# Kernel optimization log

Hardware: AMD Instinct MI355X
Metric: run time of the kernel (lower is better)

The kernel has to match this reference:

```python
import jax, jax.numpy as jnp
import numpy as np

E = 256   # embed_size
H = 256   # hidden_size
C = 3     # channels
V = 257   # pixel vocab (0..255 + boundary token 256)
B, R, CO = 128, 32, 32


def setup_inputs() -> dict:
    key = jax.random.key(0)
    ks = jax.random.split(key, 16)
    s = 0.05
    return {
        "x": jax.random.randint(ks[0], (B, C, R, CO), 0, V),
        "emb": jax.random.normal(ks[1], (C, V, E), dtype=jnp.float32) * s,
        "xcomb_W": jax.random.normal(ks[2], (C, E, 2 * E), dtype=jnp.float32) * s,
        "xcomb_b": jax.random.normal(ks[3], (C, E), dtype=jnp.float32) * s,
        "hcomb_W": jax.random.normal(ks[4], (C, H, 2 * H), dtype=jnp.float32) * s,
        "hcomb_b": jax.random.normal(ks[5], (C, H), dtype=jnp.float32) * s,
        "W_ih": jax.random.normal(ks[6], (C, 3 * H, E + 2), dtype=jnp.float32) * s,
        "W_hh": jax.random.normal(ks[7], (C, 3 * H, H), dtype=jnp.float32) * s,
        "b_ih": jax.random.normal(ks[8], (C, 3 * H), dtype=jnp.float32) * s,
        "b_hh": jax.random.normal(ks[9], (C, 3 * H), dtype=jnp.float32) * s,
        "red_W": jax.random.normal(ks[10], (V, H), dtype=jnp.float32) * s,
        "red_b": jax.random.normal(ks[11], (V,), dtype=jnp.float32) * s,
        "green_W": jax.random.normal(ks[12], (V, H + E), dtype=jnp.float32) * s,
        "green_b": jax.random.normal(ks[13], (V,), dtype=jnp.float32) * s,
        "blue_W": jax.random.normal(ks[14], (V, H + 2 * E), dtype=jnp.float32) * s,
        "blue_b": jax.random.normal(ks[15], (V,), dtype=jnp.float32) * s,
    }


def _forward(x, emb, xcomb_W, xcomb_b, hcomb_W, hcomb_b, W_ih, W_hh, b_ih, b_hh,
             red_W, red_b, green_W, green_b, blue_W, blue_b):
    Bb, Cc, Rr, Co = x.shape
    Nr, Nc = Rr - 1, Co - 1
    Hd = W_hh.shape[-1]
    dt = emb.dtype

    # context pixel indices for each output position (row+1,col+1)
    left = x[:, :, 1:, :-1]    # x[:,c,row+1,col]
    above = x[:, :, :-1, 1:]   # x[:,c,row,col+1]
    target = x[:, :, 1:, 1:]   # x[:,c,row+1,col+1] (conditioning embeds for green/blue)

    # per-channel embedding gather, vectorized over all positions
    gather = jax.vmap(lambda t, idx: t[idx], in_axes=(0, 1), out_axes=1)
    left_e = gather(emb, left)      # [B,C,Nr,Nc,E]
    above_e = gather(emb, above)
    target_e = gather(emb, target)

    # x_comb linear on cat(left,above); hidden-independent -> precompute
    xi = jnp.concatenate([left_e, above_e], axis=-1)                     # [B,C,Nr,Nc,2E]
    xi = jnp.einsum('bcrke,cfe->bcrkf', xi, xcomb_W) + xcomb_b[None, :, None, None, :]

    # positional (row,col) features appended as floats (torch.cat promotion)
    pos_r = jnp.broadcast_to(jnp.arange(Nr, dtype=dt)[:, None], (Nr, Nc))
    pos_c = jnp.broadcast_to(jnp.arange(Nc, dtype=dt)[None, :], (Nr, Nc))
    pos = jnp.broadcast_to(jnp.stack([pos_r, pos_c], -1)[None, None], (Bb, Cc, Nr, Nc, 2))
    xfull = jnp.concatenate([xi, pos], axis=-1)                          # [B,C,Nr,Nc,E+2]

    # GRU input projection is hidden-independent -> precompute gates_x
    gx = jnp.einsum('bcrkf,cgf->bcrkg', xfull, W_ih) + b_ih[None, :, None, None, :]
    gx = jnp.transpose(gx, (2, 3, 1, 0, 4))                              # [Nr,Nc,C,B,3H]

    def col_step(prev_left, xs):
        gx_col, prev_row_col = xs   # [C,B,3H], [C,B,H]
        pl = prev_left              # [B,H], shared across channels and cols
        hs = []
        for c in range(Cc):         # fixed small channel loop (sequential dependence)
            hcat = jnp.concatenate([pl, prev_row_col[c]], axis=-1)       # [B,2H]
            h = hcat @ hcomb_W[c].T + hcomb_b[c]                          # [B,H]
            gh = h @ W_hh[c].T + b_hh[c]                                  # [B,3H]
            gxr, gxz, gxn = jnp.split(gx_col[c], 3, axis=-1)
            ghr, ghz, ghn = jnp.split(gh, 3, axis=-1)
            r = jax.nn.sigmoid(gxr + ghr)
            z = jax.nn.sigmoid(gxz + ghz)
            n = jnp.tanh(gxn + r * ghn)
            hnew = (1.0 - z) * n + z * h
            pl = hnew
            hs.append(hnew)
        return pl, jnp.stack(hs, 0)  # carry, [C,B,H]

    def row_step(prev_row, gx_row):
        # prev_row: hiddens from previous row [Nc,C,B,H]
        init_left = jnp.zeros((Bb, Hd), dtype=dt)
        _, hs_row = jax.lax.scan(col_step, init_left, (gx_row, prev_row))
        return hs_row, hs_row

    init_row = jnp.zeros((Nc, Cc, Bb, Hd), dtype=dt)
    _, h_all = jax.lax.scan(row_step, init_row, gx)   # [Nr,Nc,C,B,H]

    te = jnp.transpose(target_e, (2, 3, 1, 0, 4))     # [Nr,Nc,C,B,E]
    h0, h1, h2 = h_all[:, :, 0], h_all[:, :, 1], h_all[:, :, 2]  # [Nr,Nc,B,H]
    lr = h0 @ red_W.T + red_b
    lg = jnp.concatenate([h1, te[:, :, 0]], -1) @ green_W.T + green_b
    lb = jnp.concatenate([h2, te[:, :, 0], te[:, :, 1]], -1) @ blue_W.T + blue_b
    logits = jnp.stack([lr, lg, lb], 0)               # [C,Nr,Nc,B,V]
    return jnp.transpose(logits, (3, 0, 1, 2, 4))     # [B,C,Nr,Nc,V]


def reference(x, emb, xcomb_W, xcomb_b, hcomb_W, hcomb_b, W_ih, W_hh, b_ih, b_hh,
              red_W, red_b, green_W, green_b, blue_W, blue_b):
    return _forward(x, emb, xcomb_W, xcomb_b, hcomb_W, hcomb_b, W_ih, W_hh,
                    b_ih, b_hh, red_W, red_b, green_W, green_b, blue_W, blue_b)
```

## Files before the change

kernel.cpp:

```cpp
#include <hip/hip_runtime.h>

typedef __attribute__((ext_vector_type(4))) float f32x4;
typedef __attribute__((ext_vector_type(8))) short s16x8;
typedef unsigned long long u64;

__device__ __forceinline__ unsigned short f2bf(float f) {
  union { float f; unsigned u; } v; v.f = f;
  unsigned r = v.u + 0x7fffu + ((v.u >> 16) & 1u);
  return (unsigned short)(r >> 16);
}


__global__ void prep_wbig(const float* __restrict__ hcomb_W, const float* __restrict__ hcomb_b,
                          const float* __restrict__ W_hh, const float* __restrict__ b_hh,
                          unsigned short* __restrict__ Wbig, float* __restrict__ bbig) {
  __shared__ float red[256];
  const int c = blockIdx.x, g = blockIdx.y, t = threadIdx.x;
  const float* hW = hcomb_W + (size_t)c * 256 * 512;
  unsigned short* orow = Wbig + ((size_t)c * 1024 + g) * 512;
  if (g < 256) {
    orow[t]       = f2bf(hW[(size_t)g * 512 + t]);
    orow[t + 256] = f2bf(hW[(size_t)g * 512 + t + 256]);
    if (t == 0) bbig[c * 1024 + g] = hcomb_b[c * 256 + g];
    return;
  }
  const int gp = g - 256;
  const float* wrow = W_hh + ((size_t)c * 768 + gp) * 256;
  float a0 = 0.f, a1 = 0.f;
  for (int h = 0; h < 256; h++) {
    float w = wrow[h];
    a0 += w * hW[(size_t)h * 512 + t];
    a1 += w * hW[(size_t)h * 512 + t + 256];
  }
  orow[t] = f2bf(a0); orow[t + 256] = f2bf(a1);
  red[t] = wrow[t] * hcomb_b[c * 256 + t];
  __syncthreads();
  for (int s = 128; s > 0; s >>= 1) { if (t < s) red[t] += red[t + s]; __syncthreads(); }
  if (t == 0) bbig[c * 1024 + g] = red[0] + b_hh[c * 768 + gp];
}

__global__ void prep_u(const float* __restrict__ emb, const float* __restrict__ xcomb_W,
                       float* __restrict__ Ul, float* __restrict__ Ua) {
  __shared__ float er[256];
  const int c = blockIdx.x, v = blockIdx.y, side = blockIdx.z, f = threadIdx.x;
  er[f] = emb[((size_t)c * 257 + v) * 256 + f];
  __syncthreads();
  const float* wrow = xcomb_W + ((size_t)c * 256 + f) * 512 + side * 256;
  float a = 0.f;
  for (int e = 0; e < 256; e++) a += er[e] * wrow[e];
  (side ? Ua : Ul)[((size_t)c * 257 + v) * 256 + f] = a;
}

__global__ void prep_t(const float* __restrict__ W_ih, const float* __restrict__ Ul,
                       const float* __restrict__ Ua, float* __restrict__ Tl, float* __restrict__ Ta) {
  __shared__ float ur[256];
  const int c = blockIdx.x, v = blockIdx.y, side = blockIdx.z, g = threadIdx.x;
  if (g < 256) ur[g] = (side ? Ua : Ul)[((size_t)c * 257 + v) * 256 + g];
  __syncthreads();
  const float* wrow = W_ih + ((size_t)c * 768 + g) * 258;
  float a = 0.f;
  for (int f = 0; f < 256; f++) a += ur[f] * wrow[f];
  (side ? Ta : Tl)[((size_t)c * 257 + v) * 768 + g] = a;
}

__global__ void prep_bgx(const float* __restrict__ W_ih, const float* __restrict__ xcomb_b,
                         const float* __restrict__ b_ih, float* __restrict__ bgx) {
  __shared__ float xb[256];
  const int c = blockIdx.x, g = threadIdx.x;
  if (g < 256) xb[g] = xcomb_b[c * 256 + g];
  __syncthreads();
  const float* wrow = W_ih + ((size_t)c * 768 + g) * 258;
  float a = b_ih[c * 768 + g];
  for (int f = 0; f < 256; f++) a += xb[f] * wrow[f];
  bgx[c * 768 + g] = a;
}

__global__ void prep_tgb(const float* __restrict__ emb, const float* __restrict__ green_W,
                         const float* __restrict__ blue_W,
                         float* __restrict__ TG, float* __restrict__ TB0, float* __restrict__ TB1) {
  __shared__ float er[256];
  const int v = blockIdx.x, which = blockIdx.y, u = threadIdx.x;
  const int ch = (which == 2) ? 1 : 0;
  if (u < 256) er[u] = emb[((size_t)ch * 257 + v) * 256 + u];
  __syncthreads();
  if (u >= 257) return;
  const float* W; int pitch, off; float* T;
  if (which == 0)      { W = green_W; pitch = 512; off = 256; T = TG;  }
  else if (which == 1) { W = blue_W;  pitch = 768; off = 256; T = TB0; }
  else                 { W = blue_W;  pitch = 768; off = 512; T = TB1; }
  const float* wrow = W + (size_t)u * pitch + off;
  float a = 0.f;
  for (int e = 0; e < 256; e++) a += er[e] * wrow[e];
  T[(size_t)v * 257 + u] = a;
}

__global__ void prep_w3(const float* __restrict__ red_W, const float* __restrict__ green_W,
                        const float* __restrict__ blue_W, unsigned short* __restrict__ W3) {
  const int c = blockIdx.x, v = blockIdx.y, t = threadIdx.x;
  float val = 0.f;
  if (v < 257) {
    if (c == 0)      val = red_W[(size_t)v * 256 + t];
    else if (c == 1) val = green_W[(size_t)v * 512 + t];
    else             val = blue_W[(size_t)v * 768 + t];
  }
  W3[((size_t)c * 272 + v) * 256 + t] = f2bf(val);
}

__global__ void prep_gx(const int* __restrict__ x,
                        const float* __restrict__ Tl, const float* __restrict__ Ta,
                        const float* __restrict__ bgx, const float* __restrict__ bbig,
                        const float* __restrict__ W_ih, float* __restrict__ pregx) {
  __shared__ float base[768];
  __shared__ int ix0[128], ix1[128];
  const int r = blockIdx.x, k = blockIdx.y, c = blockIdx.z, tid = threadIdx.x;
  for (int g = tid; g < 768; g += 256) {
    float v = bgx[c * 768 + g]
            + (float)r * W_ih[((size_t)c * 768 + g) * 258 + 256]
            + (float)k * W_ih[((size_t)c * 768 + g) * 258 + 257];
    if (g < 512) v += bbig[c * 1024 + 256 + g];
    base[g] = v;
  }
  if (tid < 128) {
    ix0[tid] = x[((tid * 3 + c) * 32 + (r + 1)) * 32 + k];
    ix1[tid] = x[((tid * 3 + c) * 32 + r) * 32 + (k + 1)];
  }
  __syncthreads();
  const size_t cell = ((size_t)(r * 31 + k)) * 3 + c;
  float* outp = pregx + cell * 3 * 128 * 256;
  const float* Tlc = Tl + (size_t)c * 257 * 768;
  const float* Tac = Ta + (size_t)c * 257 * 768;
  #pragma unroll 2
  for (int b = 0; b < 128; ++b) {
    const float* tl = Tlc + (size_t)ix0[b] * 768;
    const float* ta = Tac + (size_t)ix1[b] * 768;
    #pragma unroll
    for (int q = 0; q < 3; ++q) {
      const int g = q * 256 + tid;
      outp[((size_t)q * 128 + b) * 256 + tid] = tl[g] + ta[g] + base[g];
    }
  }
}

__global__ void zero_flags(int* __restrict__ f, int n) {
  int i = blockIdx.x * 256 + threadIdx.x;
  if (i < n) f[i] = 0;
}


__device__ __forceinline__ void spinwait(int* f, int target) {
  while (__hip_atomic_load(f, __ATOMIC_RELAXED, __HIP_MEMORY_SCOPE_AGENT) < target)
    __builtin_amdgcn_s_sleep(2);
}

__global__ __launch_bounds__(256, 2)
void persist_kernel(const int* __restrict__ x, float* __restrict__ hbuf,
                    const unsigned short* __restrict__ Wbig, const float* __restrict__ bbig,
                    const float* __restrict__ pregx,
                    const unsigned short* __restrict__ W3,
                    const float* __restrict__ TG, const float* __restrict__ TB0,
                    const float* __restrict__ TB1,
                    const float* __restrict__ red_b, const float* __restrict__ green_b,
                    const float* __restrict__ blue_b,
                    float* __restrict__ out, int* __restrict__ flags)
{
  __shared__ unsigned short Abuf[128 * 136];
  __shared__ int idx0[128], idx1[128];

  const int id = blockIdx.x;
  const int rlo = id & 7, slot = id >> 3;
  const int rhi = slot / 5, role = slot - 5 * rhi;
  const int r = rlo + 8 * rhi;
  if (r > 30) return;

  int* sflag = flags;
  int* eflag = flags + 124 * 31;

  const int tid = threadIdx.x;
  const int lane = tid & 63, wv = tid >> 6;
  const int quad = lane >> 4, l16 = lane & 15;

  if (role < 4) {
    const int jcol = role * 64 + wv * 16;
    const int j = jcol + l16;

    for (int L = r; L <= r + 92; ++L) {
      const int t = L - r;
      const int k = t / 3, c = t - 3 * k;
      const size_t cell = ((size_t)(r * 31 + k)) * 3 + c;
      const float* pg = pregx + cell * 3 * 128 * 256;

      f32x4 acc[8][4];
      const float bh  = bbig[c * 1024 + j];
      const float bn3 = bbig[c * 1024 + 768 + j];
      #pragma unroll
      for (int mt = 0; mt < 8; ++mt)
        #pragma unroll
        for (int i = 0; i < 4; ++i) {
          const int b = mt * 16 + quad * 4 + i;
          acc[mt][0][i] = bh;
          acc[mt][1][i] = pg[(size_t)b * 256 + j];
          acc[mt][2][i] = pg[(size_t)(128 + b) * 256 + j];
          acc[mt][3][i] = bn3;
        }

      if (tid == 0) {
        if (t >= 1) spinwait(&sflag[(L - 1) * 31 + r], 4);
        if (r >= 1) spinwait(&sflag[(L - 1) * 31 + (r - 1)], 4);
        if (t >= 3) {
          if (r < 30) spinwait(&sflag[(L - 2) * 31 + (r + 1)], 4);
          spinwait(&eflag[(L - 2) * 31 + r], 1);
        }
      }
      __syncthreads();
      __builtin_amdgcn_fence(__ATOMIC_ACQUIRE, "agent");

      const bool pl_zero = (t == 0);
      const bool a_zero  = (r == 0);
      const float* plp = hbuf + ((size_t)(r * 3 + (c == 0 ? 2 : c - 1)) * 128) * 256;
      const float* ap  = (r > 0) ? hbuf + ((size_t)((r - 1) * 3 + c) * 128) * 256 : hbuf;
      const unsigned short* Wb = Wbig + (size_t)c * 1024 * 512;

      for (int kc = 0; kc < 4; ++kc) {
        const bool from_pl = (kc < 2);
        const float* src = from_pl ? plp : ap;
        const bool zero = from_pl ? pl_zero : a_zero;
        const int colbase = from_pl ? kc * 128 : (kc - 2) * 128;
        __syncthreads();
        #pragma unroll 8
        for (int it = 0; it < 16; ++it) {
          const int li = it * 256 + tid;
          const int row = li >> 5;
          const int col = (li & 31) * 4;
          unsigned short o0 = 0, o1 = 0, o2 = 0, o3 = 0;
          if (!zero) {
            const float4 v = *(const float4*)(src + (size_t)row * 256 + colbase + col);
            o0 = f2bf(v.x); o1 = f2bf(v.y); o2 = f2bf(v.z); o3 = f2bf(v.w);
          }
          unsigned short* d = &Abuf[row * 136 + col];
          d[0] = o0; d[1] = o1; d[2] = o2; d[3] = o3;
        }
        __syncthreads();
        #pragma unroll
        for (int ks = 0; ks < 4; ++ks) {
          const int kofs = ks * 32 + quad * 8;
          s16x8 bf[4];
          #pragma unroll
          for (int g = 0; g < 4; ++g)
            bf[g] = *(const s16x8*)(Wb + (size_t)(g * 256 + jcol + l16) * 512 + kc * 128 + kofs);
          #pragma unroll
          for (int mt = 0; mt < 8; ++mt) {
            const s16x8 af = *(const s16x8*)&Abuf[(mt * 16 + l16) * 136 + kofs];
            #pragma unroll
            for (int g = 0; g < 4; ++g)
              acc[mt][g] = __builtin_amdgcn_mfma_f32_16x16x32_bf16(af, bf[g], acc[mt][g], 0, 0, 0);
          }
        }
      }

      const float* pgn = pg + (size_t)2 * 128 * 256;
      float* hout = hbuf + ((size_t)(r * 3 + c) * 128) * 256;
      #pragma unroll
      for (int mt = 0; mt < 8; ++mt)
        #pragma unroll
        for (int i = 0; i < 4; ++i) {
          const int b = mt * 16 + quad * 4 + i;
          const float gxn = pgn[(size_t)b * 256 + j];
          const float h  = acc[mt][0][i];
          const float rg = __fdividef(1.f, 1.f + __expf(-acc[mt][1][i]));
          const float zg = __fdividef(1.f, 1.f + __expf(-acc[mt][2][i]));
          const float ng = 1.f - __fdividef(2.f, __expf(2.f * (gxn + rg * acc[mt][3][i])) + 1.f);
          hout[(size_t)b * 256 + j] = (1.f - zg) * ng + zg * h;
        }

      __syncthreads();
      if (tid == 0)
        __hip_atomic_fetch_add(&sflag[L * 31 + r], 1, __ATOMIC_RELEASE, __HIP_MEMORY_SCOPE_AGENT);
    }
  } else {
    for (int Le = r + 1; Le <= r + 93; ++Le) {
      const int t = Le - 1 - r;
      const int k = t / 3, c = t - 3 * k;

      if (tid == 0) spinwait(&sflag[(Le - 1) * 31 + r], 4);
      __syncthreads();
      __builtin_amdgcn_fence(__ATOMIC_ACQUIRE, "agent");

      if (tid < 128) {
        idx0[tid] = x[((tid * 3 + 0) * 32 + (r + 1)) * 32 + (k + 1)];
        idx1[tid] = x[((tid * 3 + 1) * 32 + (r + 1)) * 32 + (k + 1)];
      }

      const float* hsrc = hbuf + ((size_t)(r * 3 + c) * 128) * 256;
      const unsigned short* W3c = W3 + (size_t)c * 272 * 256;

      f32x4 acc[2][17];
      #pragma unroll
      for (int m2 = 0; m2 < 2; ++m2)
        #pragma unroll
        for (int nt = 0; nt < 17; ++nt)
          #pragma unroll
          for (int e = 0; e < 4; ++e) acc[m2][nt][e] = 0.f;

      for (int kc = 0; kc < 2; ++kc) {
        __syncthreads();
        #pragma unroll 8
        for (int it = 0; it < 16; ++it) {
          const int li = it * 256 + tid;
          const int row = li >> 5;
          const int col = (li & 31) * 4;
          const float4 v = *(const float4*)(hsrc + (size_t)row * 256 + kc * 128 + col);
          unsigned short* d = &Abuf[row * 136 + col];
          d[0] = f2bf(v.x); d[1] = f2bf(v.y); d[2] = f2bf(v.z); d[3] = f2bf(v.w);
        }
        __syncthreads();
        if (kc == 1 && tid == 0)
          __hip_atomic_fetch_add(&eflag[Le * 31 + r], 1, __ATOMIC_RELEASE, __HIP_MEMORY_SCOPE_AGENT);
        #pragma unroll
        for (int ks = 0; ks < 4; ++ks) {
          const int kofs = ks * 32 + quad * 8;
          s16x8 af[2];
          #pragma unroll
          for (int m2 = 0; m2 < 2; ++m2)
            af[m2] = *(const s16x8*)&Abuf[((wv * 2 + m2) * 16 + l16) * 136 + kofs];
          #pragma unroll
          for (int nt = 0; nt < 17; ++nt) {
            const s16x8 bf = *(const s16x8*)(W3c + (size_t)(nt * 16 + l16) * 256 + kc * 128 + kofs);
            #pragma unroll
            for (int m2 = 0; m2 < 2; ++m2)
              acc[m2][nt] = __builtin_amdgcn_mfma_f32_16x16x32_bf16(af[m2], bf, acc[m2][nt], 0, 0, 0);
          }
        }
      }

      const float* bias = (c == 0) ? red_b : (c == 1) ? green_b : blue_b;
      #pragma unroll
      for (int m2 = 0; m2 < 2; ++m2)
        #pragma unroll
        for (int i = 0; i < 4; ++i) {
          const int b = (m2 + wv * 2) * 16 + quad * 4 + i;
          const int t0 = idx0[b], t1 = idx1[b];
          float* orow = out + ((size_t)((b * 3 + c) * 31 + r) * 31 + k) * 257;
          #pragma unroll
          for (int nt = 0; nt < 17; ++nt) {
            const int v = nt * 16 + l16;
            if (v < 257) {
              float val = acc[m2][nt][i] + bias[v];
              if (c == 1)      val += TG[(size_t)t0 * 257 + v];
              else if (c == 2) val += TB0[(size_t)t0 * 257 + v] + TB1[(size_t)t1 * 257 + v];
              orow[v] = val;
            }
          }
        }
    }
  }
}


extern "C" void kernel_launch(void* const* d_in, const int* in_sizes, int n_in,
                              void* d_out, int out_size, void* d_ws, size_t ws_size,
                              hipStream_t stream) {
  const int*   x       = (const int*)  d_in[0];
  const float* emb     = (const float*)d_in[1];
  const float* xcomb_W = (const float*)d_in[2];
  const float* xcomb_b = (const float*)d_in[3];
  const float* hcomb_W = (const float*)d_in[4];
  const float* hcomb_b = (const float*)d_in[5];
  const float* W_ih    = (const float*)d_in[6];
  const float* W_hh    = (const float*)d_in[7];
  const float* b_ih    = (const float*)d_in[8];
  const float* b_hh    = (const float*)d_in[9];
  const float* red_W   = (const float*)d_in[10];
  const float* red_b   = (const float*)d_in[11];
  const float* green_W = (const float*)d_in[12];
  const float* green_b = (const float*)d_in[13];
  const float* blue_W  = (const float*)d_in[14];
  const float* blue_b  = (const float*)d_in[15];
  float* out = (float*)d_out;

  char* p = (char*)d_ws;
  auto alloc = [&](size_t bytes) -> char* {
    char* r = p; p += (bytes + 255) & ~(size_t)255; return r;
  };
  float* hbuf          = (float*)alloc((size_t)31 * 3 * 128 * 256 * 4);
  unsigned short* Wbig = (unsigned short*)alloc((size_t)3 * 1024 * 512 * 2);
  float* bbig          = (float*)alloc((size_t)3 * 1024 * 4);
  float* Tl            = (float*)alloc((size_t)3 * 257 * 768 * 4);
  float* Ta            = (float*)alloc((size_t)3 * 257 * 768 * 4);
  float* Ul            = (float*)alloc((size_t)3 * 257 * 256 * 4);
  float* Ua            = (float*)alloc((size_t)3 * 257 * 256 * 4);
  float* bgx           = (float*)alloc((size_t)3 * 768 * 4);
  unsigned short* W3   = (unsigned short*)alloc((size_t)3 * 272 * 256 * 2);
  float* TG            = (float*)alloc((size_t)257 * 257 * 4);
  float* TB0           = (float*)alloc((size_t)257 * 257 * 4);
  float* TB1           = (float*)alloc((size_t)257 * 257 * 4);
  int*   flags         = (int*)  alloc((size_t)2 * 124 * 31 * 4);
  float* pregx         = (float*)alloc((size_t)2883 * 3 * 128 * 256 * 4);

  prep_wbig<<<dim3(3, 1024), dim3(256), 0, stream>>>(hcomb_W, hcomb_b, W_hh, b_hh, Wbig, bbig);
  prep_u<<<dim3(3, 257, 2), dim3(256), 0, stream>>>(emb, xcomb_W, Ul, Ua);
  prep_t<<<dim3(3, 257, 2), dim3(768), 0, stream>>>(W_ih, Ul, Ua, Tl, Ta);
  prep_bgx<<<dim3(3), dim3(768), 0, stream>>>(W_ih, xcomb_b, b_ih, bgx);
  prep_tgb<<<dim3(257, 3), dim3(320), 0, stream>>>(emb, green_W, blue_W, TG, TB0, TB1);
  prep_w3<<<dim3(3, 272), dim3(256), 0, stream>>>(red_W, green_W, blue_W, W3);
  prep_gx<<<dim3(31, 31, 3), dim3(256), 0, stream>>>(x, Tl, Ta, bgx, bbig, W_ih, pregx);
  zero_flags<<<dim3(31), dim3(256), 0, stream>>>(flags, 2 * 124 * 31);

  persist_kernel<<<dim3(160), dim3(256), 0, stream>>>(
      x, hbuf, Wbig, bbig, pregx, W3, TG, TB0, TB1, red_b, green_b, blue_b, out, flags);
}
```

Baseline: 10.39 ms.

## Replace agent-scope acquire fences with coherent atomic loads of hidden states

New measurement: 9.559 ms. -8.0%, faster.

```diff
diff --git a/kernel.cpp b/kernel.cpp
--- a/kernel.cpp
+++ b/kernel.cpp
@@ -152,6 +152,10 @@
     __builtin_amdgcn_s_sleep(2);
 }
 
+__device__ __forceinline__ u64 load_coh(const float* p) {
+  return __hip_atomic_load((const u64*)p, __ATOMIC_RELAXED, __HIP_MEMORY_SCOPE_SYSTEM);
+}
+
 __global__ __launch_bounds__(256, 2)
 void persist_kernel(const int* __restrict__ x, float* __restrict__ hbuf,
                     const unsigned short* __restrict__ Wbig, const float* __restrict__ bbig,
@@ -212,7 +216,7 @@
         }
       }
       __syncthreads();
-      __builtin_amdgcn_fence(__ATOMIC_ACQUIRE, "agent");
+      __builtin_amdgcn_fence(__ATOMIC_ACQUIRE, "workgroup");
 
       const bool pl_zero = (t == 0);
       const bool a_zero  = (r == 0);
@@ -231,13 +235,17 @@
           const int li = it * 256 + tid;
           const int row = li >> 5;
           const int col = (li & 31) * 4;
-          unsigned short o0 = 0, o1 = 0, o2 = 0, o3 = 0;
+          u64 q0 = 0, q1 = 0;
           if (!zero) {
-            const float4 v = *(const float4*)(src + (size_t)row * 256 + colbase + col);
-            o0 = f2bf(v.x); o1 = f2bf(v.y); o2 = f2bf(v.z); o3 = f2bf(v.w);
+            const float* sp = src + (size_t)row * 256 + colbase + col;
+            q0 = load_coh(sp);
+            q1 = load_coh(sp + 2);
           }
-          unsigned short* d = &Abuf[row * 136 + col];
-          d[0] = o0; d[1] = o1; d[2] = o2; d[3] = o3;
+          union { u64 q; float f[2]; } a0, a1; a0.q = q0; a1.q = q1;
+          union { unsigned short s[4]; u64 q; } o;
+          o.s[0] = f2bf(a0.f[0]); o.s[1] = f2bf(a0.f[1]);
+          o.s[2] = f2bf(a1.f[0]); o.s[3] = f2bf(a1.f[1]);
+          *(u64*)&Abuf[row * 136 + col] = o.q;
         }
         __syncthreads();
         #pragma unroll
@@ -281,14 +289,14 @@
       const int t = Le - 1 - r;
       const int k = t / 3, c = t - 3 * k;
 
-      if (tid == 0) spinwait(&sflag[(Le - 1) * 31 + r], 4);
-      __syncthreads();
-      __builtin_amdgcn_fence(__ATOMIC_ACQUIRE, "agent");
-
       if (tid < 128) {
         idx0[tid] = x[((tid * 3 + 0) * 32 + (r + 1)) * 32 + (k + 1)];
         idx1[tid] = x[((tid * 3 + 1) * 32 + (r + 1)) * 32 + (k + 1)];
       }
+
+      if (tid == 0) spinwait(&sflag[(Le - 1) * 31 + r], 4);
+      __syncthreads();
+      __builtin_amdgcn_fence(__ATOMIC_ACQUIRE, "workgroup");
 
       const float* hsrc = hbuf + ((size_t)(r * 3 + c) * 128) * 256;
       const unsigned short* W3c = W3 + (size_t)c * 272 * 256;
@@ -308,13 +316,18 @@
           const int li = it * 256 + tid;
           const int row = li >> 5;
           const int col = (li & 31) * 4;
-          const float4 v = *(const float4*)(hsrc + (size_t)row * 256 + kc * 128 + col);
-          unsigned short* d = &Abuf[row * 136 + col];
-          d[0] = f2bf(v.x); d[1] = f2bf(v.y); d[2] = f2bf(v.z); d[3] = f2bf(v.w);
+          const float* sp = hsrc + (size_t)row * 256 + kc * 128 + col;
+          union { u64 q; float f[2]; } a0, a1;
+          a0.q = load_coh(sp);
+          a1.q = load_coh(sp + 2);
+          union { unsigned short s[4]; u64 q; } o;
+          o.s[0] = f2bf(a0.f[0]); o.s[1] = f2bf(a0.f[1]);
+          o.s[2] = f2bf(a1.f[0]); o.s[3] = f2bf(a1.f[1]);
+          *(u64*)&Abuf[row * 136 + col] = o.q;
         }
         __syncthreads();
         if (kc == 1 && tid == 0)
-          __hip_atomic_fetch_add(&eflag[Le * 31 + r], 1, __ATOMIC_RELEASE, __HIP_MEMORY_SCOPE_AGENT);
+          __hip_atomic_fetch_add(&eflag[Le * 31 + r], 1, __ATOMIC_RELAXED, __HIP_MEMORY_SCOPE_AGENT);
         #pragma unroll
         for (int ks = 0; ks < 4; ++ks) {
           const int kofs = ks * 32 + quad * 8;
```
